# Performance work log

Hardware: AMD Instinct MI355X
Metric: run time of the kernel (lower is better)

## Reference

```python
import jax, jax.numpy as jnp
import numpy as np

H, D, KD, E = 8, 128, 16, 128
B, G = 16, 501

def setup_inputs() -> dict:
    key = jax.random.key(0)
    ks = jax.random.split(key, 12)
    stdv = 1.0 / np.sqrt(KD)
    u = lambda k, shape, s: jax.random.uniform(k, shape, jnp.float32, -s, s)
    inp = {"q": jax.random.normal(ks[0], (B, G, D), jnp.float32)}
    names = ["W_query", "W_key", "W_val", "W1_query", "W2_query", "W3_query",
             "W4_query", "W5_query", "W6_query"]
    for i, n in enumerate(names):
        inp[n] = u(ks[i + 1], (H, D, KD), stdv)
    inp["W_out"] = u(ks[10], (H, KD, E), 1.0 / np.sqrt(E))
    return inp

def _forward(q, W_query, W_key, W_val, W1, W2, W3, W4, W5, W6, W_out):
    h = q  # self-attention: h defaults to q
    b, g, d = h.shape
    np_ = (g - 1) // 2
    norm = 1.0 / jnp.sqrt(jnp.float32(KD))
    pick = h[:, 1:np_ + 1]          # [b, np, d]
    delivery = h[:, np_ + 1:]       # [b, np, d]
    proj = lambda x, W: jnp.einsum('bnd,hdk->hbnk', x, W)
    Q = proj(q, W_query); K = proj(h, W_key); V = proj(h, W_val)
    K_pick = proj(pick, W_key); V_pick = proj(pick, W_val)
    K_del = proj(delivery, W_key); V_del = proj(delivery, W_val)
    Q_pick = proj(pick, W1); Q_pick_ap = proj(pick, W2); Q_pick_ad = proj(pick, W3)
    Q_del = proj(delivery, W4); Q_del_ad = proj(delivery, W5); Q_del_ap = proj(delivery, W6)

    comp = norm * jnp.einsum('hbqk,hbgk->hbqg', Q, K)                 # [h,b,g,g]
    c_pd = norm * jnp.sum(Q_pick * K_del, -1)                          # [h,b,np]
    c_p_ap = norm * jnp.einsum('hbqk,hbpk->hbqp', Q_pick_ap, K_pick)   # [h,b,np,np]
    c_p_ad = norm * jnp.einsum('hbqk,hbpk->hbqp', Q_pick_ad, K_del)
    c_dp = norm * jnp.sum(Q_del * K_pick, -1)                          # [h,b,np]
    c_d_ad = norm * jnp.einsum('hbqk,hbpk->hbqp', Q_del_ad, K_del)
    c_d_ap = norm * jnp.einsum('hbqk,hbpk->hbqp', Q_del_ap, K_pick)

    ninf = lambda *s: jnp.full(s, -jnp.inf, comp.dtype)
    # pad branch scores to query length g (depot row + wrong-subset rows = -inf)
    c_add_del = jnp.concatenate([ninf(H, b, 1), c_pd, ninf(H, b, np_)], -1)[..., None]            # [h,b,g,1]
    c_add_ap = jnp.concatenate([ninf(H, b, 1, np_), c_p_ap, ninf(H, b, np_, np_)], 2)             # [h,b,g,np]
    c_add_ad = jnp.concatenate([ninf(H, b, 1, np_), c_p_ad, ninf(H, b, np_, np_)], 2)
    c_add_pick = jnp.concatenate([ninf(H, b, 1), ninf(H, b, np_), c_dp], -1)[..., None]
    c_add_ad2 = jnp.concatenate([ninf(H, b, 1, np_), ninf(H, b, np_, np_), c_d_ad], 2)
    c_add_ap2 = jnp.concatenate([ninf(H, b, 1, np_), ninf(H, b, np_, np_), c_d_ap], 2)
    comp_full = jnp.concatenate([comp, c_add_del, c_add_ap, c_add_ad,
                                 c_add_pick, c_add_ad2, c_add_ap2], -1)  # [h,b,g,g+2+4*np]

    attn = jax.nn.softmax(comp_full, axis=-1)

    z = lambda *s: jnp.zeros(s, V.dtype)
    V_add_del = jnp.concatenate([z(H, b, 1, KD), V_del, z(H, b, np_, KD)], 2)   # [h,b,g,kd]
    V_add_pick = jnp.concatenate([z(H, b, 1, KD), z(H, b, np_, KD), V_pick], 2)

    mm = lambda a, v: jnp.einsum('hbqp,hbpk->hbqk', a, v)
    heads = mm(attn[..., :g], V)
    heads = heads + attn[..., g:g + 1] * V_add_del
    heads = heads + mm(attn[..., g + 1:g + 1 + np_], V_pick)
    heads = heads + mm(attn[..., g + 1 + np_:g + 1 + 2 * np_], V_del)
    heads = heads + attn[..., g + 1 + 2 * np_:g + 2 + 2 * np_] * V_add_pick
    heads = heads + mm(attn[..., g + 2 + 2 * np_:g + 2 + 3 * np_], V_del)
    heads = heads + mm(attn[..., g + 2 + 3 * np_:], V_pick)

    return jnp.einsum('hbnk,hke->bne', heads, W_out)

def reference(q, W_query, W_key, W_val, W1_query, W2_query, W3_query,
              W4_query, W5_query, W6_query, W_out):
    return _forward(q, W_query, W_key, W_val, W1_query, W2_query, W3_query,
                    W4_query, W5_query, W6_query, W_out)
```

## Files before the change

### kernel.cpp

```cpp
#include <hip/hip_runtime.h>

#define H_ 8
#define D_ 128
#define KD_ 16
#define E_ 128
#define B_ 16
#define G_ 501
#define NP_ 250
#define BN_ (B_*G_)

typedef __bf16 bf16x8 __attribute__((ext_vector_type(8)));
typedef float f32x4 __attribute__((ext_vector_type(4)));
typedef unsigned short u16x8 __attribute__((ext_vector_type(8)));
typedef bf16x8 __attribute__((may_alias)) bf16x8_a;
typedef u16x8 __attribute__((may_alias)) u16x8_a;

__device__ __forceinline__ unsigned short f2bf(float f) {
  unsigned int u = __builtin_bit_cast(unsigned int, f);
  unsigned int r = u + 0x7FFFu + ((u >> 16) & 1u);
  return (unsigned short)(r >> 16);
}
__device__ __forceinline__ float bf2f(unsigned short u) {
  unsigned int v = ((unsigned int)u) << 16;
  return __builtin_bit_cast(float, v);
}
__device__ __forceinline__ int vpos(int key) {
  return (key & ~31) | ((key & 15) << 1) | ((key >> 4) & 1);
}

__global__ __launch_bounds__(256) void k_prep(
    const float* __restrict__ q,
    const float* __restrict__ w0, const float* __restrict__ w1, const float* __restrict__ w2,
    const float* __restrict__ w3, const float* __restrict__ w4, const float* __restrict__ w5,
    const float* __restrict__ w6, const float* __restrict__ w7, const float* __restrict__ w8,
    unsigned short* __restrict__ qb, unsigned short* __restrict__ wct) {
  int i = blockIdx.x * 256 + threadIdx.x;
  if (i < BN_*D_) qb[i] = f2bf(q[i]);
  if (i < H_*9*KD_*D_) {
    int d = i & 127; int t = i >> 7; int k = t & 15; t >>= 4;
    int wi = t % 9; int h = t / 9;
    const float* src = w0;
    switch (wi) {
      case 1: src = w1; break; case 2: src = w2; break; case 3: src = w3; break;
      case 4: src = w4; break; case 5: src = w5; break; case 6: src = w6; break;
      case 7: src = w7; break; case 8: src = w8; break; default: break;
    }
    wct[i] = f2bf(src[h*(D_*KD_) + d*KD_ + k]);
  }
}

__global__ __launch_bounds__(256) void k_proj(const unsigned short* __restrict__ qb,
                                              const unsigned short* __restrict__ wct,
                                              unsigned short* __restrict__ P) {
  const int tid = threadIdx.x;
  const int lane = tid & 63;
  const int wv = tid >> 6;
  const int ln = lane & 15;
  const int quad = lane >> 4;
  const int b = blockIdx.y >> 3;
  const int nt = blockIdx.y & 7;
  const int cbase = blockIdx.x * 64;

  __shared__ __align__(16) unsigned short sA[64*136];
  __shared__ __align__(16) unsigned short sB[64*136];

  for (int i = tid; i < 1024; i += 256) {
    int rr = i >> 4, half = i & 15;
    int r = min(nt*64 + rr, G_ - 1);
    u16x8 v = *(const u16x8*)(qb + (size_t)(b*G_ + r)*D_ + half*8);
    *(u16x8*)(sA + rr*136 + half*8) = v;
  }
  for (int i = tid; i < 1024; i += 256) {
    int cc = i >> 4, half = i & 15;
    u16x8 v = *(const u16x8*)(wct + (size_t)(cbase + cc)*D_ + half*8);
    *(u16x8*)(sB + cc*136 + half*8) = v;
  }
  __syncthreads();

  bf16x8 a[4];
  #pragma unroll
  for (int ks = 0; ks < 4; ++ks)
    a[ks] = *(const bf16x8_a*)(sA + (wv*16 + ln)*136 + ks*32 + quad*8);

  #pragma unroll
  for (int ct = 0; ct < 4; ++ct) {
    f32x4 acc = {0.f,0.f,0.f,0.f};
    #pragma unroll
    for (int ks = 0; ks < 4; ++ks) {
      bf16x8 bb = *(const bf16x8_a*)(sB + (ct*16 + ln)*136 + ks*32 + quad*8);
      acc = __builtin_amdgcn_mfma_f32_16x16x32_bf16(a[ks], bb, acc, 0,0,0);
    }
    const int c = cbase + ct*16 + ln;
    const int h = c / 144; const int rem = c - h*144; const int w = rem >> 4; const int k = rem & 15;
    const float sc = (w == 1 || w == 2) ? 1.0f : 0.25f;
    const size_t pb = ((size_t)((h*9 + w)*B_ + b)*G_)*KD_ + k;
    #pragma unroll
    for (int g = 0; g < 4; ++g) {
      const int nn = nt*64 + wv*16 + quad*4 + g;
      if (nn < G_) P[pb + (size_t)nn*KD_] = f2bf(acc[g]*sc);
    }
  }
}

template<bool UP, bool UD>
__device__ __forceinline__ void attn_chunk(
    int c, const unsigned short* sK, const unsigned short* sVt, unsigned int* myE,
    bf16x8 aQa, bf16x8 aQp, bf16x8 aQd,
    const float* rv, float* esum, f32x4& acc, int ln, int quad)
{
  const f32x4 z4 = {0.f,0.f,0.f,0.f};
  const unsigned short* kb = sK + c*512 + ln*16 + quad*8;
  bf16x8 bk0 = *(const bf16x8_a*)(kb);
  bf16x8 bk1 = *(const bf16x8_a*)(kb + 256);
  f32x4 sa0 = __builtin_amdgcn_mfma_f32_16x16x32_bf16(aQa, bk0, z4, 0,0,0);
  f32x4 sa1 = __builtin_amdgcn_mfma_f32_16x16x32_bf16(aQa, bk1, z4, 0,0,0);
  f32x4 sp0 = z4, sp1 = z4, sd0 = z4, sd1 = z4;
  if (UP) {
    sp0 = __builtin_amdgcn_mfma_f32_16x16x32_bf16(aQp, bk0, z4, 0,0,0);
    sp1 = __builtin_amdgcn_mfma_f32_16x16x32_bf16(aQp, bk1, z4, 0,0,0);
  }
  if (UD) {
    sd0 = __builtin_amdgcn_mfma_f32_16x16x32_bf16(aQd, bk0, z4, 0,0,0);
    sd1 = __builtin_amdgcn_mfma_f32_16x16x32_bf16(aQd, bk1, z4, 0,0,0);
  }
  const int k0 = c*32 + ln, k1 = k0 + 16;
  const float am1 = (k1 <= 500) ? 1.f : 0.f;
  const float pm0 = (k0 >= 1 && k0 <= 250) ? 1.f : 0.f;
  const float pm1 = (k1 <= 250) ? 1.f : 0.f;
  const float dm0 = (k0 >= 251) ? 1.f : 0.f;
  const float dm1 = (k1 >= 251 && k1 <= 500) ? 1.f : 0.f;
  #pragma unroll
  for (int g = 0; g < 4; ++g) {
    float e0 = __expf(sa0[g]);
    float e1 = am1 * __expf(sa1[g]);
    float x0 = 0.f, x1 = 0.f;
    if (UP) { x0 += pm0*__expf(sp0[g]); x1 += pm1*__expf(sp1[g]); }
    if (UD) { x0 += dm0*__expf(sd0[g]); x1 += dm1*__expf(sd1[g]); }
    e0 += rv[g]*x0; e1 += rv[g]*x1;
    esum[g] += e0 + e1;
    myE[(quad*4 + g)*20 + ln] = (unsigned)f2bf(e0) | ((unsigned)f2bf(e1) << 16);
  }
  bf16x8 Ef = *(const bf16x8_a*)((const unsigned short*)myE + ln*40 + quad*8);
  bf16x8 Vf = *(const bf16x8_a*)(sVt + ln*520 + c*32 + quad*8);
  acc = __builtin_amdgcn_mfma_f32_16x16x32_bf16(Ef, Vf, acc, 0,0,0);
}

__global__ __launch_bounds__(256, 3) void k_attn(const unsigned short* __restrict__ P,
                                                 float* __restrict__ heads) {
  const int rt = blockIdx.x, b = blockIdx.y, h = blockIdx.z;
  const int tid = threadIdx.x;
  const int lane = tid & 63;
  const int wv = tid >> 6;
  const int ln = lane & 15;
  const int quad = lane >> 4;
  const int r0 = rt * 64;

  __shared__ __align__(16) unsigned short sK [513*16];
  __shared__ __align__(16) unsigned short sVt[16*520];
  __shared__ __align__(16) unsigned short sQa[65*16];
  __shared__ __align__(16) unsigned short sQp[65*16];
  __shared__ __align__(16) unsigned short sQd[65*16];
  __shared__ __align__(16) unsigned short sQs[65*16];
  __shared__ __align__(16) unsigned short sKs[65*16];
  __shared__ __align__(16) unsigned int   eBuf[4*16*20];

  const size_t slab = (size_t)G_*KD_;
  const unsigned short* Pk = P + ((size_t)(h*9+1)*B_ + b)*slab;
  const unsigned short* Pv = P + ((size_t)(h*9+2)*B_ + b)*slab;
  const u16x8 vz = {0,0,0,0,0,0,0,0};

  for (int i = tid; i < 1026; i += 256) {
    int key = i >> 1;
    u16x8 v = vz;
    if (key < G_) v = *(const u16x8*)(Pk + key*KD_ + (i & 1)*8);
    *(u16x8*)(sK + i*8) = v;
  }
  for (int i = tid; i < 8192; i += 256) {
    int key = i >> 4, kd = i & 15;
    unsigned short v = (key < G_) ? Pv[key*KD_ + kd] : (unsigned short)0;
    sVt[kd*520 + vpos(key)] = v;
  }
  for (int i = tid; i < 650; i += 256) {
    int arr = i / 130;
    int j = i - arr*130;
    int rr = j >> 1, half = j & 1;
    int r = r0 + rr;
    u16x8 v = vz;
    if (rr < 64 && r < G_) {
      bool pick = (r <= NP_);
      const unsigned short* src;
      if (arr == 4) {
        int ks = (r == 0) ? 0 : (pick ? r + NP_ : r - NP_);
        src = Pk + ks*KD_;
      } else {
        int w = (arr == 0) ? 0 : (arr == 1) ? (pick ? 4 : 8)
              : (arr == 2) ? (pick ? 5 : 7) : (pick ? 3 : 6);
        src = P + ((size_t)(h*9 + w)*B_ + b)*slab + (size_t)r*KD_;
      }
      v = *(const u16x8*)(src + half*8);
    }
    unsigned short* dst = (arr==0) ? sQa : (arr==1) ? sQp : (arr==2) ? sQd
                        : (arr==3) ? sQs : sKs;
    *(u16x8*)(dst + j*8) = v;
  }
  __syncthreads();

  const int aoff = (wv*16 + ln)*16 + quad*8;
  bf16x8 aQa = *(const bf16x8_a*)(sQa + aoff);
  bf16x8 aQp = *(const bf16x8_a*)(sQp + aoff);
  bf16x8 aQd = *(const bf16x8_a*)(sQd + aoff);
  bf16x8 aQs = *(const bf16x8_a*)(sQs + aoff);
  if (quad >= 2) {
    bf16x8 zb = {};
    aQa = zb; aQp = zb; aQd = zb; aQs = zb;
  }

  const int rw0 = r0 + wv*16;
  float rv[4], rvs[4]; int posks[4];
  #pragma unroll
  for (int g = 0; g < 4; ++g) {
    int ra = rw0 + quad*4 + g;
    rv[g]  = (ra >= 1) ? 1.f : 0.f;
    rvs[g] = (ra >= 1 && ra < G_) ? 1.f : 0.f;
    int ks = (ra >= 1) ? ((ra <= NP_) ? ra + NP_ : ra - NP_) : 0;
    posks[g] = vpos(ks);
  }

  f32x4 acc = {0.f,0.f,0.f,0.f};
  float esum[4] = {0.f,0.f,0.f,0.f};
  unsigned int* myE = eBuf + wv*320;

  for (int c = 0; c < 7; ++c)
    attn_chunk<true,false>(c, sK, sVt, myE, aQa, aQp, aQd, rv, esum, acc, ln, quad);
  attn_chunk<true,true>(7, sK, sVt, myE, aQa, aQp, aQd, rv, esum, acc, ln, quad);
  for (int c = 8; c < 16; ++c)
    attn_chunk<false,true>(c, sK, sVt, myE, aQa, aQp, aQd, rv, esum, acc, ln, quad);

  const f32x4 z4 = {0.f,0.f,0.f,0.f};
  bf16x8 bks = *(const bf16x8_a*)(sKs + aoff);
  f32x4 ss = __builtin_amdgcn_mfma_f32_16x16x32_bf16(aQs, bks, z4, 0,0,0);
  float es[4];
  #pragma unroll
  for (int g = 0; g < 4; ++g) {
    float v = __shfl(ss[g], quad*16 + quad*4 + g, 64);
    es[g] = rvs[g] * __expf(v);
  }
  #pragma unroll
  for (int g = 0; g < 4; ++g) {
    float t = esum[g];
    t += __shfl_xor(t, 1); t += __shfl_xor(t, 2);
    t += __shfl_xor(t, 4); t += __shfl_xor(t, 8);
    esum[g] = t + es[g];
  }
  #pragma unroll
  for (int g = 0; g < 4; ++g) {
    int ra = rw0 + quad*4 + g;
    float o = acc[g] + es[g] * bf2f(sVt[ln*520 + posks[g]]);
    if (ra < G_)
      heads[((size_t)(b*G_ + ra))*E_ + h*16 + ln] = o * __builtin_amdgcn_rcpf(esum[g]);
  }
}

__global__ __launch_bounds__(256) void k_out(const float* __restrict__ heads,
                                             const float* __restrict__ wout,
                                             float* __restrict__ out) {
  const int base = blockIdx.x * 16;
  const int tid = threadIdx.x;
  __shared__ __align__(16) float sA[16*128];
  for (int i = tid; i < 512; i += 256)
    ((float4*)sA)[i] = ((const float4*)heads)[(size_t)base*32 + i];
  __syncthreads();
  const int cg = tid & 31, rh = tid >> 5;
  float4 acc0 = make_float4(0.f,0.f,0.f,0.f);
  float4 acc1 = make_float4(0.f,0.f,0.f,0.f);
  const float4* w4 = (const float4*)wout;
  #pragma unroll 8
  for (int kk = 0; kk < 128; ++kk) {
    float4 wv = w4[kk*32 + cg];
    float a0 = sA[(rh*2)*128 + kk];
    float a1 = sA[(rh*2+1)*128 + kk];
    acc0.x = fmaf(a0, wv.x, acc0.x); acc0.y = fmaf(a0, wv.y, acc0.y);
    acc0.z = fmaf(a0, wv.z, acc0.z); acc0.w = fmaf(a0, wv.w, acc0.w);
    acc1.x = fmaf(a1, wv.x, acc1.x); acc1.y = fmaf(a1, wv.y, acc1.y);
    acc1.z = fmaf(a1, wv.z, acc1.z); acc1.w = fmaf(a1, wv.w, acc1.w);
  }
  ((float4*)out)[(size_t)(base + rh*2)*32 + cg] = acc0;
  ((float4*)out)[(size_t)(base + rh*2 + 1)*32 + cg] = acc1;
}

extern "C" void kernel_launch(void* const* d_in, const int* in_sizes, int n_in,
                              void* d_out, int out_size, void* d_ws, size_t ws_size,
                              hipStream_t stream) {
  const float* q = (const float*)d_in[0];
  const float* w0 = (const float*)d_in[1];
  const float* w1 = (const float*)d_in[2];
  const float* w2 = (const float*)d_in[3];
  const float* w3 = (const float*)d_in[4];
  const float* w4 = (const float*)d_in[5];
  const float* w5 = (const float*)d_in[6];
  const float* w6 = (const float*)d_in[7];
  const float* w7 = (const float*)d_in[8];
  const float* w8 = (const float*)d_in[9];
  const float* wout = (const float*)d_in[10];
  float* out = (float*)d_out;

  char* ws = (char*)d_ws;
  unsigned short* qb  = (unsigned short*)(ws);
  unsigned short* wct = (unsigned short*)(ws + 2052096);
  unsigned short* P   = (unsigned short*)(ws + 2347008);
  float* heads        = (float*)(ws + 20815872);

  k_prep<<<dim3(4008), dim3(256), 0, stream>>>(q, w0,w1,w2,w3,w4,w5,w6,w7,w8, qb, wct);
  k_proj<<<dim3(18, 128), dim3(256), 0, stream>>>(qb, wct, P);
  k_attn<<<dim3(8, 16, 8), dim3(256), 0, stream>>>(P, heads);
  k_out<<<dim3(501), dim3(256), 0, stream>>>(heads, wout, out);
}
```

Before: 141.7 us.

## Fuse q bf16 conversion into projection and restructure attention score loop

The separate q-to-bf16 conversion pass is removed: k_proj now reads fp32 q and converts while staging it into shared memory, so one full read/write of q through global memory goes away. The attention kernel is reorganised to compute transposed scores (K as the A operand), which removes the V position swizzle. It also double-buffers the exp tile so two chunks are scored before their PV MFMAs, replaces the single-key MFMA plus shuffle with a scalar dot product, and writes outputs as float4. The masking logic is rewritten per chunk, and the larger exp buffer raises shared-memory use.

```diff
diff --git a/kernel.cpp b/kernel.cpp
--- a/kernel.cpp
+++ b/kernel.cpp
@@ -12,8 +12,10 @@
 typedef __bf16 bf16x8 __attribute__((ext_vector_type(8)));
 typedef float f32x4 __attribute__((ext_vector_type(4)));
 typedef unsigned short u16x8 __attribute__((ext_vector_type(8)));
+typedef unsigned short u16x4 __attribute__((ext_vector_type(4)));
 typedef bf16x8 __attribute__((may_alias)) bf16x8_a;
 typedef u16x8 __attribute__((may_alias)) u16x8_a;
+typedef u16x4 __attribute__((may_alias)) u16x4_a;
 
 __device__ __forceinline__ unsigned short f2bf(float f) {
   unsigned int u = __builtin_bit_cast(unsigned int, f);
@@ -24,18 +26,13 @@
   unsigned int v = ((unsigned int)u) << 16;
   return __builtin_bit_cast(float, v);
 }
-__device__ __forceinline__ int vpos(int key) {
-  return (key & ~31) | ((key & 15) << 1) | ((key >> 4) & 1);
-}
 
 __global__ __launch_bounds__(256) void k_prep(
-    const float* __restrict__ q,
     const float* __restrict__ w0, const float* __restrict__ w1, const float* __restrict__ w2,
     const float* __restrict__ w3, const float* __restrict__ w4, const float* __restrict__ w5,
     const float* __restrict__ w6, const float* __restrict__ w7, const float* __restrict__ w8,
-    unsigned short* __restrict__ qb, unsigned short* __restrict__ wct) {
+    unsigned short* __restrict__ wct) {
   int i = blockIdx.x * 256 + threadIdx.x;
-  if (i < BN_*D_) qb[i] = f2bf(q[i]);
   if (i < H_*9*KD_*D_) {
     int d = i & 127; int t = i >> 7; int k = t & 15; t >>= 4;
     int wi = t % 9; int h = t / 9;
@@ -49,7 +46,7 @@
   }
 }
 
-__global__ __launch_bounds__(256) void k_proj(const unsigned short* __restrict__ qb,
+__global__ __launch_bounds__(256) void k_proj(const float* __restrict__ q,
                                               const unsigned short* __restrict__ wct,
                                               unsigned short* __restrict__ P) {
   const int tid = threadIdx.x;
@@ -67,7 +64,12 @@
   for (int i = tid; i < 1024; i += 256) {
     int rr = i >> 4, half = i & 15;
     int r = min(nt*64 + rr, G_ - 1);
-    u16x8 v = *(const u16x8*)(qb + (size_t)(b*G_ + r)*D_ + half*8);
+    const float* src = q + (size_t)(b*G_ + r)*D_ + half*8;
+    float4 f0 = ((const float4*)src)[0];
+    float4 f1 = ((const float4*)src)[1];
+    u16x8 v;
+    v[0]=f2bf(f0.x); v[1]=f2bf(f0.y); v[2]=f2bf(f0.z); v[3]=f2bf(f0.w);
+    v[4]=f2bf(f1.x); v[5]=f2bf(f1.y); v[6]=f2bf(f1.z); v[7]=f2bf(f1.w);
     *(u16x8*)(sA + rr*136 + half*8) = v;
   }
   for (int i = tid; i < 1024; i += 256) {
@@ -102,47 +104,60 @@
   }
 }
 
-template<bool UP, bool UD>
-__device__ __forceinline__ void attn_chunk(
-    int c, const unsigned short* sK, const unsigned short* sVt, unsigned int* myE,
-    bf16x8 aQa, bf16x8 aQp, bf16x8 aQd,
-    const float* rv, float* esum, f32x4& acc, int ln, int quad)
+__device__ __forceinline__ f32x4 mf(bf16x8 a, bf16x8 b, f32x4 c) {
+  return __builtin_amdgcn_mfma_f32_16x16x32_bf16(a, b, c, 0,0,0);
+}
+
+__device__ __forceinline__ void score_chunk(
+    int c, bool up, bool dn, int cbuf,
+    const unsigned short* sK, bf16x8 qa, bf16x8 qp, bf16x8 qdl,
+    unsigned short* eb, float rv, float& esum, int ln, int quad)
 {
   const f32x4 z4 = {0.f,0.f,0.f,0.f};
-  const unsigned short* kb = sK + c*512 + ln*16 + quad*8;
-  bf16x8 bk0 = *(const bf16x8_a*)(kb);
-  bf16x8 bk1 = *(const bf16x8_a*)(kb + 256);
-  f32x4 sa0 = __builtin_amdgcn_mfma_f32_16x16x32_bf16(aQa, bk0, z4, 0,0,0);
-  f32x4 sa1 = __builtin_amdgcn_mfma_f32_16x16x32_bf16(aQa, bk1, z4, 0,0,0);
+  bf16x8 k0 = {}, k1 = {};
+  if (quad < 2) {
+    const unsigned short* kp = sK + (c*32 + ln)*16 + quad*8;
+    k0 = *(const bf16x8_a*)(kp);
+    k1 = *(const bf16x8_a*)(kp + 256);
+  }
+  f32x4 sa0 = mf(k0, qa, z4), sa1 = mf(k1, qa, z4);
   f32x4 sp0 = z4, sp1 = z4, sd0 = z4, sd1 = z4;
-  if (UP) {
-    sp0 = __builtin_amdgcn_mfma_f32_16x16x32_bf16(aQp, bk0, z4, 0,0,0);
-    sp1 = __builtin_amdgcn_mfma_f32_16x16x32_bf16(aQp, bk1, z4, 0,0,0);
-  }
-  if (UD) {
-    sd0 = __builtin_amdgcn_mfma_f32_16x16x32_bf16(aQd, bk0, z4, 0,0,0);
-    sd1 = __builtin_amdgcn_mfma_f32_16x16x32_bf16(aQd, bk1, z4, 0,0,0);
-  }
-  const int k0 = c*32 + ln, k1 = k0 + 16;
-  const float am1 = (k1 <= 500) ? 1.f : 0.f;
-  const float pm0 = (k0 >= 1 && k0 <= 250) ? 1.f : 0.f;
-  const float pm1 = (k1 <= 250) ? 1.f : 0.f;
-  const float dm0 = (k0 >= 251) ? 1.f : 0.f;
-  const float dm1 = (k1 >= 251 && k1 <= 500) ? 1.f : 0.f;
-  #pragma unroll
-  for (int g = 0; g < 4; ++g) {
-    float e0 = __expf(sa0[g]);
-    float e1 = am1 * __expf(sa1[g]);
-    float x0 = 0.f, x1 = 0.f;
-    if (UP) { x0 += pm0*__expf(sp0[g]); x1 += pm1*__expf(sp1[g]); }
-    if (UD) { x0 += dm0*__expf(sd0[g]); x1 += dm1*__expf(sd1[g]); }
-    e0 += rv[g]*x0; e1 += rv[g]*x1;
-    esum[g] += e0 + e1;
-    myE[(quad*4 + g)*20 + ln] = (unsigned)f2bf(e0) | ((unsigned)f2bf(e1) << 16);
-  }
-  bf16x8 Ef = *(const bf16x8_a*)((const unsigned short*)myE + ln*40 + quad*8);
-  bf16x8 Vf = *(const bf16x8_a*)(sVt + ln*520 + c*32 + quad*8);
-  acc = __builtin_amdgcn_mfma_f32_16x16x32_bf16(Ef, Vf, acc, 0,0,0);
+  if (up) { sp0 = mf(k0, qp, z4);  sp1 = mf(k1, qp, z4); }
+  if (dn) { sd0 = mf(k0, qdl, z4); sd1 = mf(k1, qdl, z4); }
+
+  float el = 0.f;
+  unsigned short ev[8];
+  #pragma unroll
+  for (int t = 0; t < 2; ++t) {
+    #pragma unroll
+    for (int rg = 0; rg < 4; ++rg) {
+      float comp = __expf(t ? sa1[rg] : sa0[rg]);
+      if (c == 15 && t == 1) comp *= (quad*4 + rg <= 4) ? 1.f : 0.f;
+      float ex = 0.f;
+      if (up) {
+        float m = 1.f;
+        if (c == 0 && t == 0 && rg == 0) m = (quad != 0) ? 1.f : 0.f;
+        if (c == 7 && t == 1) m = (quad*4 + rg <= 10) ? 1.f : 0.f;
+        ex += m * __expf(t ? sp1[rg] : sp0[rg]);
+      }
+      if (dn) {
+        float m = 1.f;
+        if (c == 7)  m = (t == 1 && quad*4 + rg >= 11) ? 1.f : 0.f;
+        if (c == 15 && t == 1) m = (quad*4 + rg <= 4) ? 1.f : 0.f;
+        ex += m * __expf(t ? sd1[rg] : sd0[rg]);
+      }
+      float e = comp + rv * ex;
+      el += e;
+      ev[t*4 + rg] = f2bf(e);
+    }
+  }
+  esum += el;
+  u16x4 w0, w1;
+  w0[0]=ev[0]; w0[1]=ev[1]; w0[2]=ev[2]; w0[3]=ev[3];
+  w1[0]=ev[4]; w1[1]=ev[5]; w1[2]=ev[6]; w1[3]=ev[7];
+  unsigned short* base = eb + cbuf*640 + ln*40 + quad*4;
+  *(u16x4_a*)(base)      = w0;
+  *(u16x4_a*)(base + 16) = w1;
 }
 
 __global__ __launch_bounds__(256, 3) void k_attn(const unsigned short* __restrict__ P,
@@ -155,21 +170,21 @@
   const int quad = lane >> 4;
   const int r0 = rt * 64;
 
-  __shared__ __align__(16) unsigned short sK [513*16];
+  __shared__ __align__(16) unsigned short sK [512*16];
   __shared__ __align__(16) unsigned short sVt[16*520];
   __shared__ __align__(16) unsigned short sQa[65*16];
   __shared__ __align__(16) unsigned short sQp[65*16];
   __shared__ __align__(16) unsigned short sQd[65*16];
   __shared__ __align__(16) unsigned short sQs[65*16];
   __shared__ __align__(16) unsigned short sKs[65*16];
-  __shared__ __align__(16) unsigned int   eBuf[4*16*20];
+  __shared__ __align__(16) unsigned short eBuf[4*2*640];
 
   const size_t slab = (size_t)G_*KD_;
   const unsigned short* Pk = P + ((size_t)(h*9+1)*B_ + b)*slab;
   const unsigned short* Pv = P + ((size_t)(h*9+2)*B_ + b)*slab;
   const u16x8 vz = {0,0,0,0,0,0,0,0};
 
-  for (int i = tid; i < 1026; i += 256) {
+  for (int i = tid; i < 1024; i += 256) {
     int key = i >> 1;
     u16x8 v = vz;
     if (key < G_) v = *(const u16x8*)(Pk + key*KD_ + (i & 1)*8);
@@ -177,8 +192,7 @@
   }
   for (int i = tid; i < 8192; i += 256) {
     int key = i >> 4, kd = i & 15;
-    unsigned short v = (key < G_) ? Pv[key*KD_ + kd] : (unsigned short)0;
-    sVt[kd*520 + vpos(key)] = v;
+    sVt[kd*520 + key] = (key < G_) ? Pv[key*KD_ + kd] : (unsigned short)0;
   }
   for (int i = tid; i < 650; i += 256) {
     int arr = i / 130;
@@ -206,59 +220,57 @@
   __syncthreads();
 
   const int aoff = (wv*16 + ln)*16 + quad*8;
-  bf16x8 aQa = *(const bf16x8_a*)(sQa + aoff);
-  bf16x8 aQp = *(const bf16x8_a*)(sQp + aoff);
-  bf16x8 aQd = *(const bf16x8_a*)(sQd + aoff);
-  bf16x8 aQs = *(const bf16x8_a*)(sQs + aoff);
-  if (quad >= 2) {
-    bf16x8 zb = {};
-    aQa = zb; aQp = zb; aQd = zb; aQs = zb;
-  }
+  bf16x8 qa  = *(const bf16x8_a*)(sQa + aoff);
+  bf16x8 qp  = *(const bf16x8_a*)(sQp + aoff);
+  bf16x8 qdl = *(const bf16x8_a*)(sQd + aoff);
 
   const int rw0 = r0 + wv*16;
-  float rv[4], rvs[4]; int posks[4];
-  #pragma unroll
-  for (int g = 0; g < 4; ++g) {
-    int ra = rw0 + quad*4 + g;
-    rv[g]  = (ra >= 1) ? 1.f : 0.f;
-    rvs[g] = (ra >= 1 && ra < G_) ? 1.f : 0.f;
-    int ks = (ra >= 1) ? ((ra <= NP_) ? ra + NP_ : ra - NP_) : 0;
-    posks[g] = vpos(ks);
-  }
+  const int ra = rw0 + ln;
+  const float rv = (ra >= 1) ? 1.f : 0.f;
+  unsigned short* eb = eBuf + wv*1280;
 
   f32x4 acc = {0.f,0.f,0.f,0.f};
-  float esum[4] = {0.f,0.f,0.f,0.f};
-  unsigned int* myE = eBuf + wv*320;
-
-  for (int c = 0; c < 7; ++c)
-    attn_chunk<true,false>(c, sK, sVt, myE, aQa, aQp, aQd, rv, esum, acc, ln, quad);
-  attn_chunk<true,true>(7, sK, sVt, myE, aQa, aQp, aQd, rv, esum, acc, ln, quad);
-  for (int c = 8; c < 16; ++c)
-    attn_chunk<false,true>(c, sK, sVt, myE, aQa, aQp, aQd, rv, esum, acc, ln, quad);
-
-  const f32x4 z4 = {0.f,0.f,0.f,0.f};
-  bf16x8 bks = *(const bf16x8_a*)(sKs + aoff);
-  f32x4 ss = __builtin_amdgcn_mfma_f32_16x16x32_bf16(aQs, bks, z4, 0,0,0);
-  float es[4];
-  #pragma unroll
-  for (int g = 0; g < 4; ++g) {
-    float v = __shfl(ss[g], quad*16 + quad*4 + g, 64);
-    es[g] = rvs[g] * __expf(v);
-  }
-  #pragma unroll
-  for (int g = 0; g < 4; ++g) {
-    float t = esum[g];
-    t += __shfl_xor(t, 1); t += __shfl_xor(t, 2);
-    t += __shfl_xor(t, 4); t += __shfl_xor(t, 8);
-    esum[g] = t + es[g];
-  }
-  #pragma unroll
-  for (int g = 0; g < 4; ++g) {
-    int ra = rw0 + quad*4 + g;
-    float o = acc[g] + es[g] * bf2f(sVt[ln*520 + posks[g]]);
-    if (ra < G_)
-      heads[((size_t)(b*G_ + ra))*E_ + h*16 + ln] = o * __builtin_amdgcn_rcpf(esum[g]);
-  }
+  float esum = 0.f;
+
+  #pragma unroll
+  for (int p = 0; p < 8; ++p) {
+    const int c0 = 2*p, c1 = c0 + 1;
+    score_chunk(c0, c0 <= 7, c0 >= 7, 0, sK, qa, qp, qdl, eb, rv, esum, ln, quad);
+    score_chunk(c1, c1 <= 7, c1 >= 7, 1, sK, qa, qp, qdl, eb, rv, esum, ln, quad);
+    #pragma unroll
+    for (int u = 0; u < 2; ++u) {
+      bf16x8 Ef = *(const bf16x8_a*)(eb + u*640 + ln*40 + quad*8);
+      bf16x8 Vf = *(const bf16x8_a*)(sVt + ln*520 + (c0+u)*32 + quad*8);
+      acc = mf(Vf, Ef, acc);
+    }
+  }
+
+  esum += __shfl_xor(esum, 16);
+  esum += __shfl_xor(esum, 32);
+
+  const unsigned short* qsp = sQs + (wv*16 + ln)*16;
+  const unsigned short* ksp = sKs + (wv*16 + ln)*16;
+  u16x8 qs0 = *(const u16x8_a*)(qsp), qs1 = *(const u16x8_a*)(qsp + 8);
+  u16x8 ks0 = *(const u16x8_a*)(ksp), ks1 = *(const u16x8_a*)(ksp + 8);
+  float s = 0.f;
+  #pragma unroll
+  for (int kd = 0; kd < 8; ++kd) {
+    s = fmaf(bf2f(qs0[kd]), bf2f(ks0[kd]), s);
+    s = fmaf(bf2f(qs1[kd]), bf2f(ks1[kd]), s);
+  }
+  const float rvs = (ra >= 1 && ra < G_) ? 1.f : 0.f;
+  const float esng = rvs * __expf(s);
+  esum += esng;
+  const int kpair = (ra >= 1 && ra < G_) ? ((ra <= NP_) ? ra + NP_ : ra - NP_) : 0;
+
+  const float rcp = __builtin_amdgcn_rcpf(esum);
+  float4 o;
+  o.x = (acc[0] + esng * bf2f(sVt[(quad*4+0)*520 + kpair])) * rcp;
+  o.y = (acc[1] + esng * bf2f(sVt[(quad*4+1)*520 + kpair])) * rcp;
+  o.z = (acc[2] + esng * bf2f(sVt[(quad*4+2)*520 + kpair])) * rcp;
+  o.w = (acc[3] + esng * bf2f(sVt[(quad*4+3)*520 + kpair])) * rcp;
+  if (ra < G_)
+    *(float4*)(heads + ((size_t)(b*G_ + ra))*E_ + h*16 + quad*4) = o;
 }
 
 __global__ __launch_bounds__(256) void k_out(const float* __restrict__ heads,
@@ -305,13 +317,12 @@
   float* out = (float*)d_out;
 
   char* ws = (char*)d_ws;
-  unsigned short* qb  = (unsigned short*)(ws);
-  unsigned short* wct = (unsigned short*)(ws + 2052096);
-  unsigned short* P   = (unsigned short*)(ws + 2347008);
-  float* heads        = (float*)(ws + 20815872);
-
-  k_prep<<<dim3(4008), dim3(256), 0, stream>>>(q, w0,w1,w2,w3,w4,w5,w6,w7,w8, qb, wct);
-  k_proj<<<dim3(18, 128), dim3(256), 0, stream>>>(qb, wct, P);
+  unsigned short* wct = (unsigned short*)(ws);
+  unsigned short* P   = (unsigned short*)(ws + 294912);
+  float* heads        = (float*)(ws + 18763776);
+
+  k_prep<<<dim3(4608), dim3(256), 0, stream>>>(w0,w1,w2,w3,w4,w5,w6,w7,w8, wct);
+  k_proj<<<dim3(18, 128), dim3(256), 0, stream>>>(q, wct, P);
   k_attn<<<dim3(8, 16, 8), dim3(256), 0, stream>>>(P, heads);
   k_out<<<dim3(501), dim3(256), 0, stream>>>(heads, wout, out);
 }
```

New measurement: 144.0 us. No clear change (+1.6%).
